# Kernel tuning notes

Measured on AMD Instinct MI355X. Metric: run time of the kernel, lower is better.

The kernel has to match this reference:

```python
import jax, jax.numpy as jnp
import numpy as np

EPS = 1e-5
K = 16

gelu = lambda x: jax.nn.gelu(x, approximate=False)

def _ln(x, g, b):
    mu = jnp.mean(x, -1, keepdims=True)
    var = jnp.mean((x - mu) ** 2, -1, keepdims=True)
    return (x - mu) * jax.lax.rsqrt(var + EPS) * g + b

def _bn_last(x, g, b, m, v):  # BN over channels-last axis (eval mode, running stats)
    return (x - m) * jax.lax.rsqrt(v + EPS) * g + b

def _bn_c(x, g, b, m, v):  # x [B,C,T]
    return (x - m[None, :, None]) * jax.lax.rsqrt(v + EPS)[None, :, None] * g[None, :, None] + b[None, :, None]

def _conv1d(x, w, b, pad):  # x [B,C,T], w [O,I,W]
    y = jax.lax.conv_general_dilated(x, w, (1,), [(pad, pad)], dimension_numbers=('NCH', 'OIH', 'NCH'))
    return y + b[None, :, None]

def _edge_conv(x, ew1, eg1, eb1, em1, ev1, ew2, eg2, eb2, em2, ev2):
    # x: [BT,P,C]; kNN in xyz (first 3 channels), gather neighbors, edge MLP, max over k
    xyz = x[..., :3]
    sq = jnp.sum(xyz * xyz, -1)
    d = sq[:, :, None] + sq[:, None, :] - 2.0 * jnp.einsum('bpc,bqc->bpq', xyz, xyz)
    _, idx = jax.lax.top_k(-d, K)                       # k smallest distances (incl. self)
    x_j = jax.vmap(lambda xb, ib: xb[ib])(x, idx)       # [BT,P,K,C]
    x_i = jnp.broadcast_to(x[:, :, None, :], x_j.shape)
    edge = jnp.concatenate([x_i, x_j - x_i], -1)        # [BT,P,K,2C]
    h = gelu(_bn_last(jnp.einsum('bpke,oe->bpko', edge, ew1), eg1, eb1, em1, ev1))
    h = gelu(_bn_last(jnp.einsum('bpko,qo->bpkq', h, ew2), eg2, eb2, em2, ev2))
    return jnp.max(h, axis=2)                           # [BT,P,128]

def setup_inputs():
    key = jax.random.key(0)
    ks = iter(jax.random.split(key, 80))
    def r(shape, s=0.05):
        return jax.random.normal(next(ks), shape, jnp.float32) * s
    d = {}
    d['x_pt'] = jax.random.normal(next(ks), (8, 32, 256, 10), jnp.float32)
    d['x_fr'] = jax.random.normal(next(ks), (8, 32, 4), jnp.float32)
    d['ew1'] = r((64, 20), 0.1)
    d['eg1'], d['eb1'], d['em1'], d['ev1'] = jnp.ones(64), jnp.zeros(64), r((64,)), jnp.ones(64)
    d['ew2'] = r((128, 64), 0.1)
    d['eg2'], d['eb2'], d['em2'], d['ev2'] = jnp.ones(128), jnp.zeros(128), r((128,)), jnp.ones(128)
    d['p1w'], d['p1b'] = r((138, 128), 0.08), r((128,))
    d['ln1g'], d['ln1b'] = jnp.ones(128), jnp.zeros(128)
    d['p2w'], d['p2b'] = r((128, 256), 0.08), r((256,))
    d['ln2g'], d['ln2b'] = jnp.ones(256), jnp.zeros(256)
    d['f1w'], d['f1b'] = r((4, 32), 0.3), r((32,))
    d['f2w'], d['f2b'] = r((32, 64), 0.15), r((64,))
    d['projw'], d['projb'] = r((256, 576, 1), 0.04), r((256,))
    for i in (1, 2, 3, 4):
        d['c%dw' % i], d['c%db' % i] = r((256, 256, 3), 0.03), r((256,))
        d['g%d' % i], d['be%d' % i], d['m%d' % i], d['v%d' % i] = jnp.ones(256), jnp.zeros(256), r((256,)), jnp.ones(256)
    d['h1w'], d['h1b'] = r((256, 128), 0.08), r((128,))
    d['h2w'], d['h2b'] = r((128, 25), 0.08), r((25,))
    return d

def reference(x_pt, x_fr, ew1, eg1, eb1, em1, ev1, ew2, eg2, eb2, em2, ev2, p1w, p1b, ln1g, ln1b, p2w, p2b, ln2g, ln2b, f1w, f1b, f2w, f2b, projw, projb, c1w, c1b, g1, be1, m1, v1, c2w, c2b, g2, be2, m2, v2, c3w, c3b, g3, be3, m3, v3, c4w, c4b, g4, be4, m4, v4, h1w, h1b, h2w, h2b):
    B, T, P, C = x_pt.shape
    x_bt = x_pt.reshape(B * T, P, C)
    local = _edge_conv(x_bt, ew1, eg1, eb1, em1, ev1, ew2, eg2, eb2, em2, ev2)
    h = jnp.concatenate([local, x_bt], -1)              # [BT,P,138]
    h = gelu(_ln(h @ p1w + p1b, ln1g, ln1b))
    h = gelu(_ln(h @ p2w + p2b, ln2g, ln2b))
    h = h.reshape(B, T, P, 256)
    pf = jnp.concatenate([jnp.max(h, 2), jnp.mean(h, 2)], -1)  # [B,T,512]
    fr = gelu(x_fr @ f1w + f1b) @ f2w + f2b                    # [B,T,64]
    per = jnp.concatenate([pf, fr], -1)                        # [B,T,576]
    hs = jnp.transpose(per, (0, 2, 1))                         # [B,576,T]
    hs = _conv1d(hs, projw, projb, 0)
    hs = gelu(_bn_c(_conv1d(hs, c1w, c1b, 1), g1, be1, m1, v1))
    hs = hs + gelu(_bn_c(_conv1d(hs, c2w, c2b, 1), g2, be2, m2, v2))
    hs = hs + gelu(_bn_c(_conv1d(hs, c3w, c3b, 1), g3, be3, m3, v3))
    hs = hs + gelu(_bn_c(_conv1d(hs, c4w, c4b, 1), g4, be4, m4, v4))
    pooled = jnp.max(hs, -1)                                   # [B,256]
    return gelu(pooled @ h1w + h1b) @ h2w + h2b                # [B,25]
```

## Files before the change

kernel.cpp:

```cpp
#include <hip/hip_runtime.h>
#include <math.h>

#define NBT   256
#define NP    256
#define NC    10
#define KNN   16
#define NPB   8

typedef unsigned short ushort_t;
typedef unsigned char uchar_t;
typedef __attribute__((ext_vector_type(8))) short short8;
typedef __attribute__((ext_vector_type(4))) float f32x4;

__device__ __forceinline__ float gelu_f(float x) {
  return 0.5f * x * (1.0f + erff(x * 0.7071067811865476f));
}
__device__ __forceinline__ float gelu_fast(float x) {
  float u  = x * 0.7071067811865476f;
  float au = fabsf(u);
  float t  = __builtin_amdgcn_rcpf(fmaf(0.3275911f, au, 1.0f));
  float p  = fmaf(t, 1.061405429f, -1.453152027f);
  p = fmaf(t, p, 1.421413741f);
  p = fmaf(t, p, -0.284496736f);
  p = fmaf(t, p, 0.254829592f);
  p = p * t;
  float e  = __expf(-au * au);
  float er = fmaf(-p, e, 1.0f);
  er = copysignf(er, u);
  return 0.5f * x * (1.0f + er);
}
__device__ __forceinline__ ushort_t f2bf(float f) {
  unsigned u = __float_as_uint(f);
  return (ushort_t)((u + 0x7FFFu + ((u >> 16) & 1u)) >> 16);
}

__global__ __launch_bounds__(256) void knn_kernel(const float* __restrict__ x_pt,
                                                  uchar_t* __restrict__ idx) {
  __shared__ float sx[NP], sy[NP], sz[NP], ssq[NP];
  int bt = blockIdx.x >> 6;
  int p0 = (blockIdx.x & 63) * 4;
  int tid = threadIdx.x;
  const float* xb = x_pt + (size_t)bt * NP * NC;
  {
    int q = tid;
    float x0 = xb[q*NC+0], x1 = xb[q*NC+1], x2 = xb[q*NC+2];
    sx[q] = x0; sy[q] = x1; sz[q] = x2;
    ssq[q] = x0*x0 + x1*x1 + x2*x2;
  }
  __syncthreads();

  int wv = tid >> 6, lane = tid & 63;
  int p = p0 + wv;
  float px = sx[p], py = sy[p], pz = sz[p], psq = ssq[p];

  unsigned k0, k1, k2, k3;
  {
    unsigned kk[4];
#pragma unroll
    for (int c = 0; c < 4; ++c) {
      int q = lane + c*64;
      float d = psq + ssq[q] - 2.0f*(px*sx[q] + py*sy[q] + pz*sz[q]);
      d = fmaxf(d, 0.0f);
      kk[c] = (__float_as_uint(d) & 0xFFFFFF00u) | (unsigned)q;
    }
    unsigned a0 = min(kk[0], kk[1]), a1 = max(kk[0], kk[1]);
    unsigned a2 = min(kk[2], kk[3]), a3 = max(kk[2], kk[3]);
    unsigned b0 = min(a0, a2), b2 = max(a0, a2);
    unsigned b1 = min(a1, a3), b3 = max(a1, a3);
    k0 = b0; k1 = min(b1, b2); k2 = max(b1, b2); k3 = b3;
  }

  unsigned cur = k0, mykeep = 0u;
#pragma unroll
  for (int r = 0; r < 16; ++r) {
    unsigned w = cur;
    w = min(w, (unsigned)__shfl_xor((int)w, 1));
    w = min(w, (unsigned)__shfl_xor((int)w, 2));
    w = min(w, (unsigned)__shfl_xor((int)w, 4));
    w = min(w, (unsigned)__shfl_xor((int)w, 8));
    w = min(w, (unsigned)__shfl_xor((int)w, 16));
    w = min(w, (unsigned)__shfl_xor((int)w, 32));
    bool win = (cur == w);
    cur = win ? k1 : cur;
    k1  = win ? k2 : k1;
    k2  = win ? k3 : k2;
    k3  = win ? 0xFFFFFFFFu : k3;
    if (lane == r) mykeep = w;
  }
  if (lane < 16)
    idx[((size_t)bt*NP + p)*KNN + lane] = (uchar_t)(mykeep & 0xFFu);
}

__global__ __launch_bounds__(256) void featAB_kernel(const float* __restrict__ x_pt,
                                                     const float* __restrict__ ew1,
                                                     float* __restrict__ Af,
                                                     float* __restrict__ Bf) {
  int t = blockIdx.x*256 + threadIdx.x;
  int o = t & 63, p = t >> 6;
  const float* xr = x_pt + (size_t)p*NC;
  float a = 0.f, b = 0.f;
#pragma unroll
  for (int e = 0; e < NC; ++e) {
    float w1 = ew1[o*20 + e], w2 = ew1[o*20 + 10 + e];
    float xv = xr[e];
    a = fmaf(xv, w1 - w2, a);
    b = fmaf(xv, w2, b);
  }
  Af[(size_t)p*64 + o] = a;
  Bf[(size_t)p*64 + o] = b;
}

__global__ __launch_bounds__(256) void prep_kernel(
    const float* __restrict__ p1w, const float* __restrict__ p2w,
    const float* __restrict__ ew2,
    ushort_t* __restrict__ w1b, ushort_t* __restrict__ w2b,
    ushort_t* __restrict__ ew2b) {
  int i = blockIdx.x*256 + threadIdx.x;
  if (i < 21504) {
    int o = i / 168, e = i - o*168;
    w1b[i] = f2bf((e < 138) ? p1w[e*128 + o] : 0.f);
  } else if (i < 56320) {
    int j = i - 21504;
    int q = j / 136, e = j - q*136;
    w2b[j] = f2bf((e < 128) ? p2w[e*256 + q] : 0.f);
  } else {
    int m = i - 56320;
    int q = m / 72, o = m - q*72;
    ew2b[m] = f2bf((o < 64) ? ew2[q*64 + o] : 0.f);
  }
}

__global__ __launch_bounds__(256) void prep2_kernel(
    const float* __restrict__ projw,
    const float* __restrict__ cw0, const float* __restrict__ cw1,
    const float* __restrict__ cw2, const float* __restrict__ cw3,
    const float* __restrict__ cb0, const float* __restrict__ cb1,
    const float* __restrict__ cb2, const float* __restrict__ cb3,
    const float* __restrict__ cg0, const float* __restrict__ cg1,
    const float* __restrict__ cg2, const float* __restrict__ cg3,
    const float* __restrict__ be0, const float* __restrict__ be1,
    const float* __restrict__ be2, const float* __restrict__ be3,
    const float* __restrict__ cm0, const float* __restrict__ cm1,
    const float* __restrict__ cm2, const float* __restrict__ cm3,
    const float* __restrict__ cv0, const float* __restrict__ cv1,
    const float* __restrict__ cv2, const float* __restrict__ cv3,
    ushort_t* __restrict__ pjb, ushort_t* __restrict__ cwb,
    float* __restrict__ SCt, float* __restrict__ SHt) {
  const float* cwp[4] = {cw0, cw1, cw2, cw3};
  const float* cbp[4] = {cb0, cb1, cb2, cb3};
  const float* cgp[4] = {cg0, cg1, cg2, cg3};
  const float* bep[4] = {be0, be1, be2, be3};
  const float* cmp[4] = {cm0, cm1, cm2, cm3};
  const float* cvp[4] = {cv0, cv1, cv2, cv3};
  int i = blockIdx.x*256 + threadIdx.x;
  if (i < 147456) {
    pjb[i] = f2bf(projw[i]);
  } else if (i < 147456 + 786432) {
    int j = i - 147456;
    int lay = j / 196608, rem = j - lay*196608;
    int c = rem / 768, kp = rem - c*768;
    int dt = kp >> 8, cin = kp & 255;
    cwb[j] = f2bf(cwp[lay][c*768 + cin*3 + dt]);
  } else if (i < 147456 + 786432 + 1024) {
    int j = i - 147456 - 786432;
    int lay = j >> 8, c = j & 255;
    float rsv = 1.0f / sqrtf(cvp[lay][c] + 1e-5f);
    float sc = cgp[lay][c] * rsv;
    SCt[j] = sc;
    SHt[j] = (cbp[lay][c] - cmp[lay][c]) * sc + bep[lay][c];
  }
}

__global__ __launch_bounds__(256, 2) void edgeconv_kernel(
    const float* __restrict__ Af, const float* __restrict__ Bf,
    const uchar_t* __restrict__ idx, const ushort_t* __restrict__ ew2b,
    const float* __restrict__ eg1, const float* __restrict__ eb1,
    const float* __restrict__ em1, const float* __restrict__ ev1,
    const float* __restrict__ eg2, const float* __restrict__ eb2,
    const float* __restrict__ em2, const float* __restrict__ ev2,
    ushort_t* __restrict__ localfb) {
  __shared__ __align__(16) ushort_t h1s[128*72];
  __shared__ __align__(16) ushort_t w2T[128*72];
  __shared__ float sc1[64], sh1[64], sc2[128], sh2[128];
  __shared__ int idxs[128];

  int tid = threadIdx.x;
  int bid = blockIdx.x;
  int wid = (bid & 7) * 1024 + (bid >> 3);
  int p0  = wid * NPB;
  int bt  = p0 >> 8;

  for (int i = tid; i < 1152; i += 256)
    ((uint4*)w2T)[i] = ((const uint4*)ew2b)[i];
  if (tid < 128) idxs[tid] = idx[(size_t)p0*16 + tid];
  if (tid < 64) {
    float s = eg1[tid] * (1.0f / sqrtf(ev1[tid] + 1e-5f));
    sc1[tid] = s; sh1[tid] = eb1[tid] - em1[tid]*s;
  }
  if (tid >= 64 && tid < 192) {
    int q = tid - 64;
    float s = eg2[q] * (1.0f / sqrtf(ev2[q] + 1e-5f));
    sc2[q] = s; sh2[q] = eb2[q] - em2[q]*s;
  }
  __syncthreads();

  {
    int o = tid & 63, g = tid >> 6;
    float s1 = sc1[o], h1v = sh1[o];
    const float* Bbase = Bf + (size_t)bt*NP*64 + o;
#pragma unroll
    for (int pi = 0; pi < 2; ++pi) {
      int pt = g*2 + pi;
      float af = Af[((size_t)(p0+pt))*64 + o];
      ushort_t* hrow = h1s + (pt*16)*72 + o;
#pragma unroll
      for (int k = 0; k < KNN; ++k) {
        int j = idxs[pt*16 + k];
        float hv = af + Bbase[(size_t)j*64];
        hrow[k*72] = f2bf(gelu_fast(fmaf(hv, s1, h1v)));
      }
    }
  }
  __syncthreads();

  int w = tid >> 6, l = tid & 63;
  int m_lo = l & 15, kq = l >> 4;

  short8 afr[2][2];
#pragma unroll
  for (int pt = 0; pt < 2; ++pt)
#pragma unroll
    for (int ks = 0; ks < 2; ++ks)
      afr[pt][ks] = *(const short8*)&h1s[((2*w+pt)*16 + m_lo)*72 + ks*32 + kq*8];

  f32x4 acc[2][8];
#pragma unroll
  for (int pt = 0; pt < 2; ++pt)
#pragma unroll
    for (int ct = 0; ct < 8; ++ct) acc[pt][ct] = (f32x4){0.f,0.f,0.f,0.f};

#pragma unroll
  for (int ct = 0; ct < 8; ++ct) {
#pragma unroll
    for (int ks = 0; ks < 2; ++ks) {
      short8 bfr = *(const short8*)&w2T[(ct*16 + m_lo)*72 + ks*32 + kq*8];
      acc[0][ct] = __builtin_amdgcn_mfma_f32_16x16x32_bf16(afr[0][ks], bfr, acc[0][ct], 0, 0, 0);
      acc[1][ct] = __builtin_amdgcn_mfma_f32_16x16x32_bf16(afr[1][ks], bfr, acc[1][ct], 0, 0, 0);
    }
  }

#pragma unroll
  for (int pt = 0; pt < 2; ++pt) {
    int gp = p0 + 2*w + pt;
#pragma unroll
    for (int ct = 0; ct < 8; ++ct) {
      int q = ct*16 + m_lo;
      float sc = sc2[q], sh = sh2[q];
      f32x4 a = acc[pt][ct];
      float mn = INFINITY, mx = -INFINITY;
#pragma unroll
      for (int r = 0; r < 4; ++r) {
        float y = fmaf(a[r], sc, sh);
        mn = fminf(mn, y); mx = fmaxf(mx, y);
      }
      mn = fminf(mn, __shfl_xor(mn, 16));
      mn = fminf(mn, __shfl_xor(mn, 32));
      mx = fmaxf(mx, __shfl_xor(mx, 16));
      mx = fmaxf(mx, __shfl_xor(mx, 32));
      float g = gelu_fast((kq & 1) ? mx : mn);
      g = fmaxf(g, __shfl_xor(g, 16));
      if (l < 16)
        localfb[(size_t)gp*128 + q] = f2bf(g);
    }
  }
}

__global__ __launch_bounds__(256, 2) void p1p2_kernel(
    const ushort_t* __restrict__ localfb, const float* __restrict__ x_pt,
    const ushort_t* __restrict__ w1b, const ushort_t* __restrict__ w2b,
    const float* __restrict__ p1b,
    const float* __restrict__ ln1g, const float* __restrict__ ln1b,
    const float* __restrict__ p2b,
    const float* __restrict__ ln2g, const float* __restrict__ ln2b,
    float* __restrict__ pmaxb, float* __restrict__ psumb) {
  __shared__ __align__(16) ushort_t sA[64*168];
  __shared__ __align__(16) ushort_t wt[128*168];
  __shared__ float pm4[4*256], ps4[4*256];
  int blk = blockIdx.x;
  int bt = blk >> 2, ch = blk & 3;
  int tid = threadIdx.x;
  size_t gbase = (size_t)bt*NP + ch*64;

  for (int i = tid; i < 1024; i += 256) {
    int pp = i >> 4, v = i & 15;
    *(uint4*)(sA + pp*168 + v*8) =
        *(const uint4*)(localfb + (gbase+pp)*128 + v*8);
  }
  for (int i = tid; i < 64*40; i += 256) {
    int pp = i / 40, e = i - pp*40;
    ushort_t v = 0;
    if (e < 10) v = f2bf(x_pt[(gbase+pp)*NC + e]);
    sA[pp*168 + 128 + e] = v;
  }
  for (int i = tid; i < 2688; i += 256)
    ((uint4*)wt)[i] = ((const uint4*)w1b)[i];
  __syncthreads();

  int w = tid >> 6, l = tid & 63;
  int lo = l & 15, kq = l >> 4;

  short8 af1[5];
#pragma unroll
  for (int ks = 0; ks < 5; ++ks)
    af1[ks] = *(const short8*)&sA[(w*16 + lo)*168 + ks*32 + kq*8];
  f32x4 acc1[8];
#pragma unroll
  for (int ct = 0; ct < 8; ++ct) {
    float b = p1b[ct*16 + lo];
    acc1[ct] = (f32x4){b, b, b, b};
  }
#pragma unroll
  for (int ct = 0; ct < 8; ++ct) {
#pragma unroll
    for (int ks = 0; ks < 5; ++ks) {
      short8 bf = *(const short8*)&wt[(ct*16 + lo)*168 + ks*32 + kq*8];
      acc1[ct] = __builtin_amdgcn_mfma_f32_16x16x32_bf16(af1[ks], bf, acc1[ct], 0, 0, 0);
    }
  }
  __syncthreads();

  {
    float g1v[8], b1v[8];
#pragma unroll
    for (int ct = 0; ct < 8; ++ct) { g1v[ct] = ln1g[ct*16+lo]; b1v[ct] = ln1b[ct*16+lo]; }
#pragma unroll
    for (int r = 0; r < 4; ++r) {
      float s = 0.f;
#pragma unroll
      for (int ct = 0; ct < 8; ++ct) s += acc1[ct][r];
      s += __shfl_xor(s,1); s += __shfl_xor(s,2); s += __shfl_xor(s,4); s += __shfl_xor(s,8);
      float mu = s * (1.0f/128.0f);
      float s2 = 0.f;
#pragma unroll
      for (int ct = 0; ct < 8; ++ct) { float d = acc1[ct][r]-mu; s2 += d*d; }
      s2 += __shfl_xor(s2,1); s2 += __shfl_xor(s2,2); s2 += __shfl_xor(s2,4); s2 += __shfl_xor(s2,8);
      float rs = 1.0f / sqrtf(s2*(1.0f/128.0f) + 1e-5f);
      int row = w*16 + kq*4 + r;
#pragma unroll
      for (int ct = 0; ct < 8; ++ct) {
        float h = gelu_fast((acc1[ct][r]-mu)*rs*g1v[ct] + b1v[ct]);
        sA[row*168 + ct*16 + lo] = f2bf(h);
      }
    }
  }
  for (int i = tid; i < 2176; i += 256)
    ((uint4*)wt)[i] = ((const uint4*)w2b)[i];
  __syncthreads();

  short8 af2[4];
#pragma unroll
  for (int ks = 0; ks < 4; ++ks)
    af2[ks] = *(const short8*)&sA[(w*16 + lo)*168 + ks*32 + kq*8];
  f32x4 acc2[16];
#pragma unroll
  for (int ct = 0; ct < 8; ++ct) {
    float bA = p2b[ct*16 + lo], bB = p2b[128 + ct*16 + lo];
    acc2[ct]   = (f32x4){bA, bA, bA, bA};
    acc2[8+ct] = (f32x4){bB, bB, bB, bB};
  }
#pragma unroll
  for (int ct = 0; ct < 8; ++ct) {
#pragma unroll
    for (int ks = 0; ks < 4; ++ks) {
      short8 bf = *(const short8*)&wt[(ct*16 + lo)*136 + ks*32 + kq*8];
      acc2[ct] = __builtin_amdgcn_mfma_f32_16x16x32_bf16(af2[ks], bf, acc2[ct], 0, 0, 0);
    }
  }
  __syncthreads();
  for (int i = tid; i < 2176; i += 256)
    ((uint4*)wt)[i] = ((const uint4*)(w2b + 17408))[i];
  __syncthreads();
#pragma unroll
  for (int ct = 0; ct < 8; ++ct) {
#pragma unroll
    for (int ks = 0; ks < 4; ++ks) {
      short8 bf = *(const short8*)&wt[(ct*16 + lo)*136 + ks*32 + kq*8];
      acc2[8+ct] = __builtin_amdgcn_mfma_f32_16x16x32_bf16(af2[ks], bf, acc2[8+ct], 0, 0, 0);
    }
  }

  float vmax[16], vsum[16];
  {
    float g2v[16], b2v[16];
#pragma unroll
    for (int j = 0; j < 16; ++j) {
      int c = (j >= 8 ? 128 : 0) + (j & 7)*16 + lo;
      g2v[j] = ln2g[c]; b2v[j] = ln2b[c];
    }
#pragma unroll
    for (int j = 0; j < 16; ++j) { vmax[j] = -INFINITY; vsum[j] = 0.f; }
#pragma unroll
    for (int r = 0; r < 4; ++r) {
      float s = 0.f;
#pragma unroll
      for (int j = 0; j < 16; ++j) s += acc2[j][r];
      s += __shfl_xor(s,1); s += __shfl_xor(s,2); s += __shfl_xor(s,4); s += __shfl_xor(s,8);
      float mu = s * (1.0f/256.0f);
      float s2 = 0.f;
#pragma unroll
      for (int j = 0; j < 16; ++j) { float d = acc2[j][r]-mu; s2 += d*d; }
      s2 += __shfl_xor(s2,1); s2 += __shfl_xor(s2,2); s2 += __shfl_xor(s2,4); s2 += __shfl_xor(s2,8);
      float rs = 1.0f / sqrtf(s2*(1.0f/256.0f) + 1e-5f);
#pragma unroll
      for (int j = 0; j < 16; ++j) {
        float v = gelu_fast((acc2[j][r]-mu)*rs*g2v[j] + b2v[j]);
        vmax[j] = fmaxf(vmax[j], v);
        vsum[j] += v;
      }
    }
  }
#pragma unroll
  for (int j = 0; j < 16; ++j) {
    float m = vmax[j], s = vsum[j];
    m = fmaxf(m, __shfl_xor(m, 16)); m = fmaxf(m, __shfl_xor(m, 32));
    s += __shfl_xor(s, 16);          s += __shfl_xor(s, 32);
    if (l < 16) {
      int c = (j >= 8 ? 128 : 0) + (j & 7)*16 + l;
      pm4[w*256 + c] = m;
      ps4[w*256 + c] = s;
    }
  }
  __syncthreads();
  {
    int c = tid;
    float mx = fmaxf(fmaxf(pm4[c], pm4[256+c]), fmaxf(pm4[512+c], pm4[768+c]));
    float sm = ps4[c] + ps4[256+c] + ps4[512+c] + ps4[768+c];
    pmaxb[(size_t)blk*256 + c] = mx;
    psumb[(size_t)blk*256 + c] = sm;
  }
}

__global__ __launch_bounds__(256) void p1p2_reduce_kernel(
    const float* __restrict__ pmaxb, const float* __restrict__ psumb,
    const float* __restrict__ xfr, const float* __restrict__ f1w,
    const float* __restrict__ f1b, const float* __restrict__ f2w,
    const float* __restrict__ f2b, float* __restrict__ perbuf) {
  int bt = blockIdx.x, q = threadIdx.x;
  const float* mb = pmaxb + (size_t)bt*4*256 + q;
  const float* sb = psumb + (size_t)bt*4*256 + q;
  float mx = -INFINITY, sm = 0.f;
#pragma unroll
  for (int i = 0; i < 4; ++i) {
    mx = fmaxf(mx, mb[i*256]);
    sm += sb[i*256];
  }
  perbuf[(size_t)bt*576 + q] = mx;
  perbuf[(size_t)bt*576 + 256 + q] = sm * (1.0f/256.0f);

  if (q < 64) {
    float x0 = xfr[bt*4], x1 = xfr[bt*4+1], x2 = xfr[bt*4+2], x3 = xfr[bt*4+3];
    float acc = f2b[q];
#pragma unroll
    for (int e = 0; e < 32; ++e) {
      float hv = f1b[e];
      hv = fmaf(x0, f1w[e], hv);
      hv = fmaf(x1, f1w[32+e], hv);
      hv = fmaf(x2, f1w[64+e], hv);
      hv = fmaf(x3, f1w[96+e], hv);
      acc = fmaf(gelu_f(hv), f2w[e*64 + q], acc);
    }
    perbuf[(size_t)bt*576 + 512 + q] = acc;
  }
}

__global__ __launch_bounds__(512, 1) void tail_kernel(
    const float* __restrict__ perbuf,
    const ushort_t* __restrict__ pjb, const ushort_t* __restrict__ cwb,
    const float* __restrict__ projb,
    const float* __restrict__ SCt, const float* __restrict__ SHt,
    const float* __restrict__ h1w, const float* __restrict__ h1b,
    const float* __restrict__ h2w, const float* __restrict__ h2b,
    float* __restrict__ out) {
  __shared__ __align__(16) ushort_t perA[32*584];
  __shared__ __align__(16) float master[32*260];
  __shared__ __align__(16) ushort_t hsb[34*264];
  __shared__ float pooled[256], hh[128];
  int b = blockIdx.x, tid = threadIdx.x;
  int w = tid >> 6, l = tid & 63;
  int lo = l & 15, kq = l >> 4;
  int mt = w & 1, nq = w >> 1;

  for (int i = tid; i < 4608; i += 512) {
    int t = i / 144, v = i - t*144;
    float4 f4 = *(const float4*)(perbuf + ((size_t)b*32 + t)*576 + v*4);
    ushort_t* dst = perA + t*584 + v*4;
    dst[0]=f2bf(f4.x); dst[1]=f2bf(f4.y); dst[2]=f2bf(f4.z); dst[3]=f2bf(f4.w);
  }
  for (int i = tid; i < 264; i += 512) { hsb[i] = 0; hsb[33*264 + i] = 0; }
  __syncthreads();

  {
    f32x4 acc[4];
#pragma unroll
    for (int j = 0; j < 4; ++j) {
      float bb = projb[(nq*4+j)*16 + lo];
      acc[j] = (f32x4){bb, bb, bb, bb};
    }
    for (int ks = 0; ks < 18; ++ks) {
      short8 af = *(const short8*)&perA[(mt*16 + lo)*584 + ks*32 + kq*8];
#pragma unroll
      for (int j = 0; j < 4; ++j) {
        int ct = nq*4 + j;
        short8 bf = *(const short8*)&pjb[(ct*16 + lo)*576 + ks*32 + kq*8];
        acc[j] = __builtin_amdgcn_mfma_f32_16x16x32_bf16(af, bf, acc[j], 0, 0, 0);
      }
    }
#pragma unroll
    for (int j = 0; j < 4; ++j) {
      int col = (nq*4+j)*16 + lo;
#pragma unroll
      for (int r = 0; r < 4; ++r)
        master[(mt*16 + kq*4 + r)*260 + col] = acc[j][r];
    }
  }
  __syncthreads();

  for (int lay = 0; lay < 4; ++lay) {
    for (int i = tid; i < 8192; i += 512) {
      int t = i >> 8, c = i & 255;
      hsb[(t+1)*264 + c] = f2bf(master[t*260 + c]);
    }
    __syncthreads();

    f32x4 acc[4];
#pragma unroll
    for (int j = 0; j < 4; ++j) acc[j] = (f32x4){0.f,0.f,0.f,0.f};
    const ushort_t* wb = cwb + (size_t)lay*196608;
    for (int ks = 0; ks < 24; ++ks) {
      int dt = ks >> 3, cin0 = (ks & 7)*32 + kq*8;
      short8 af = *(const short8*)&hsb[(mt*16 + lo + dt)*264 + cin0];
#pragma unroll
      for (int j = 0; j < 4; ++j) {
        int ct = nq*4 + j;
        short8 bf = *(const short8*)&wb[(ct*16 + lo)*768 + ks*32 + kq*8];
        acc[j] = __builtin_amdgcn_mfma_f32_16x16x32_bf16(af, bf, acc[j], 0, 0, 0);
      }
    }
    __syncthreads();
#pragma unroll
    for (int j = 0; j < 4; ++j) {
      int col = (nq*4+j)*16 + lo;
      float sc = SCt[lay*256 + col], sh = SHt[lay*256 + col];
#pragma unroll
      for (int r = 0; r < 4; ++r) {
        int row = mt*16 + kq*4 + r;
        float y = gelu_fast(fmaf(acc[j][r], sc, sh));
        if (lay > 0) y += master[row*260 + col];
        master[row*260 + col] = y;
      }
    }
    __syncthreads();
  }

  if (tid < 256) {
    float mx = -INFINITY;
#pragma unroll 8
    for (int t = 0; t < 32; ++t) mx = fmaxf(mx, master[t*260 + tid]);
    pooled[tid] = mx;
  }
  __syncthreads();
  if (tid < 128) {
    float acc = h1b[tid];
    for (int e = 0; e < 256; ++e) acc = fmaf(pooled[e], h1w[e*128 + tid], acc);
    hh[tid] = gelu_f(acc);
  }
  __syncthreads();
  if (tid < 25) {
    float acc = h2b[tid];
    for (int e = 0; e < 128; ++e) acc = fmaf(hh[e], h2w[e*25 + tid], acc);
    out[b*25 + tid] = acc;
  }
}

extern "C" void kernel_launch(void* const* d_in, const int* in_sizes, int n_in,
                              void* d_out, int out_size, void* d_ws, size_t ws_size,
                              hipStream_t stream) {
  const float* x_pt = (const float*)d_in[0];
  const float* x_fr = (const float*)d_in[1];
  const float* ew1  = (const float*)d_in[2];
  const float* eg1  = (const float*)d_in[3];
  const float* eb1  = (const float*)d_in[4];
  const float* em1  = (const float*)d_in[5];
  const float* ev1  = (const float*)d_in[6];
  const float* ew2  = (const float*)d_in[7];
  const float* eg2  = (const float*)d_in[8];
  const float* eb2  = (const float*)d_in[9];
  const float* em2  = (const float*)d_in[10];
  const float* ev2  = (const float*)d_in[11];
  const float* p1w  = (const float*)d_in[12];
  const float* p1b  = (const float*)d_in[13];
  const float* ln1g = (const float*)d_in[14];
  const float* ln1b = (const float*)d_in[15];
  const float* p2w  = (const float*)d_in[16];
  const float* p2b  = (const float*)d_in[17];
  const float* ln2g = (const float*)d_in[18];
  const float* ln2b = (const float*)d_in[19];
  const float* f1w  = (const float*)d_in[20];
  const float* f1b  = (const float*)d_in[21];
  const float* f2w  = (const float*)d_in[22];
  const float* f2b  = (const float*)d_in[23];
  const float* projw= (const float*)d_in[24];
  const float* projb= (const float*)d_in[25];
  const float* cw[4] = {(const float*)d_in[26],(const float*)d_in[32],(const float*)d_in[38],(const float*)d_in[44]};
  const float* cb[4] = {(const float*)d_in[27],(const float*)d_in[33],(const float*)d_in[39],(const float*)d_in[45]};
  const float* cg[4] = {(const float*)d_in[28],(const float*)d_in[34],(const float*)d_in[40],(const float*)d_in[46]};
  const float* cbe[4]= {(const float*)d_in[29],(const float*)d_in[35],(const float*)d_in[41],(const float*)d_in[47]};
  const float* cm[4] = {(const float*)d_in[30],(const float*)d_in[36],(const float*)d_in[42],(const float*)d_in[48]};
  const float* cv[4] = {(const float*)d_in[31],(const float*)d_in[37],(const float*)d_in[43],(const float*)d_in[49]};
  const float* h1w  = (const float*)d_in[50];
  const float* h1b  = (const float*)d_in[51];
  const float* h2w  = (const float*)d_in[52];
  const float* h2b  = (const float*)d_in[53];
  float* out = (float*)d_out;

  char* ws = (char*)d_ws;
  uchar_t* idxw  = (uchar_t*)ws;
  float* perbuf  = (float*)ws;
  ushort_t* ew2b = (ushort_t*)(ws + 0x200000);
  ushort_t* w1b  = (ushort_t*)(ws + 0x200000 + 0x8000);
  ushort_t* w2b  = (ushort_t*)(ws + 0x200000 + 0x14000);
  ushort_t* pjb  = (ushort_t*)(ws + 0x200000 + 0x28000);
  ushort_t* cwb  = (ushort_t*)(ws + 0x200000 + 0x70000);
  float* SCt     = (float*)(ws + 0x200000 + 0x1F0000);
  float* SHt     = (float*)(ws + 0x200000 + 0x1F1000);
  float* pmaxb   = (float*)(ws + ((size_t)4  << 20));
  float* psumb   = (float*)(ws + ((size_t)6  << 20));
  float* Af      = (float*)(ws + ((size_t)12 << 20));
  float* Bfw     = (float*)(ws + ((size_t)28 << 20));
  ushort_t* localfb = (ushort_t*)(ws + ((size_t)44 << 20));

  knn_kernel<<<NBT*64, 256, 0, stream>>>(x_pt, idxw);
  featAB_kernel<<<(NBT*NP*64)/256, 256, 0, stream>>>(x_pt, ew1, Af, Bfw);
  prep_kernel<<<256, 256, 0, stream>>>(p1w, p2w, ew2, w1b, w2b, ew2b);
  prep2_kernel<<<3656, 256, 0, stream>>>(projw,
      cw[0], cw[1], cw[2], cw[3], cb[0], cb[1], cb[2], cb[3],
      cg[0], cg[1], cg[2], cg[3], cbe[0], cbe[1], cbe[2], cbe[3],
      cm[0], cm[1], cm[2], cm[3], cv[0], cv[1], cv[2], cv[3],
      pjb, cwb, SCt, SHt);
  edgeconv_kernel<<<(NBT*NP)/NPB, 256, 0, stream>>>(Af, Bfw, idxw, ew2b,
      eg1, eb1, em1, ev1, eg2, eb2, em2, ev2, localfb);
  p1p2_kernel<<<NBT*4, 256, 0, stream>>>(localfb, x_pt, w1b, w2b, p1b,
      ln1g, ln1b, p2b, ln2g, ln2b, pmaxb, psumb);
  p1p2_reduce_kernel<<<NBT, 256, 0, stream>>>(pmaxb, psumb, x_fr,
      f1w, f1b, f2w, f2b, perbuf);
  tail_kernel<<<8, 512, 0, stream>>>(perbuf, pjb, cwb, projb, SCt, SHt,
      h1w, h1b, h2w, h2b, out);
}
```

Before: 518.3 us.

## Split temporal conv tail across time chunks with halo recompute and separate pool/head kernel

The tail conv stack used to run on only 8 blocks, one per batch element. It now runs on 32 blocks, each handling an 8-step time chunk plus a 4-step halo on each side, so the four k=3 convs can be recomputed locally without any cross-block sync. Out-of-range timesteps are zeroed to reproduce the per-layer zero padding. Max-pooling and the MLP head move into a new small kernel, with the first head layer split across thread pairs. This costs one extra launch, redundant halo compute, and a global round-trip of the hidden states.

```diff
diff --git a/kernel.cpp b/kernel.cpp
--- a/kernel.cpp
+++ b/kernel.cpp
@@ -473,87 +473,94 @@
   }
 }
 
-__global__ __launch_bounds__(512, 1) void tail_kernel(
+__global__ __launch_bounds__(512, 1) void tail2_kernel(
     const float* __restrict__ perbuf,
     const ushort_t* __restrict__ pjb, const ushort_t* __restrict__ cwb,
     const float* __restrict__ projb,
     const float* __restrict__ SCt, const float* __restrict__ SHt,
-    const float* __restrict__ h1w, const float* __restrict__ h1b,
-    const float* __restrict__ h2w, const float* __restrict__ h2b,
-    float* __restrict__ out) {
-  __shared__ __align__(16) ushort_t perA[32*584];
-  __shared__ __align__(16) float master[32*260];
-  __shared__ __align__(16) ushort_t hsb[34*264];
-  __shared__ float pooled[256], hh[128];
-  int b = blockIdx.x, tid = threadIdx.x;
+    float* __restrict__ hs4) {
+  __shared__ __align__(16) ushort_t perA[16*584];
+  __shared__ __align__(16) float master[16*260];
+  __shared__ __align__(16) ushort_t hsb[18*264];
+  int blk = blockIdx.x;
+  int b = blk >> 2, chunk = blk & 3;
+  int w0 = chunk*8 - 4;
+  int tid = threadIdx.x;
   int w = tid >> 6, l = tid & 63;
   int lo = l & 15, kq = l >> 4;
-  int mt = w & 1, nq = w >> 1;
-
-  for (int i = tid; i < 4608; i += 512) {
+
+  for (int i = tid; i < 16*144; i += 512) {
     int t = i / 144, v = i - t*144;
-    float4 f4 = *(const float4*)(perbuf + ((size_t)b*32 + t)*576 + v*4);
+    int gt = w0 + t;
     ushort_t* dst = perA + t*584 + v*4;
-    dst[0]=f2bf(f4.x); dst[1]=f2bf(f4.y); dst[2]=f2bf(f4.z); dst[3]=f2bf(f4.w);
-  }
-  for (int i = tid; i < 264; i += 512) { hsb[i] = 0; hsb[33*264 + i] = 0; }
+    if (gt >= 0 && gt < 32) {
+      float4 f4 = *(const float4*)(perbuf + ((size_t)b*32 + gt)*576 + v*4);
+      dst[0]=f2bf(f4.x); dst[1]=f2bf(f4.y); dst[2]=f2bf(f4.z); dst[3]=f2bf(f4.w);
+    } else {
+      dst[0]=0; dst[1]=0; dst[2]=0; dst[3]=0;
+    }
+  }
+  for (int i = tid; i < 264; i += 512) { hsb[i] = 0; hsb[17*264 + i] = 0; }
   __syncthreads();
 
   {
-    f32x4 acc[4];
-#pragma unroll
-    for (int j = 0; j < 4; ++j) {
-      float bb = projb[(nq*4+j)*16 + lo];
+    f32x4 acc[2];
+#pragma unroll
+    for (int j = 0; j < 2; ++j) {
+      float bb = projb[(2*w+j)*16 + lo];
       acc[j] = (f32x4){bb, bb, bb, bb};
     }
     for (int ks = 0; ks < 18; ++ks) {
-      short8 af = *(const short8*)&perA[(mt*16 + lo)*584 + ks*32 + kq*8];
-#pragma unroll
-      for (int j = 0; j < 4; ++j) {
-        int ct = nq*4 + j;
-        short8 bf = *(const short8*)&pjb[(ct*16 + lo)*576 + ks*32 + kq*8];
+      short8 af = *(const short8*)&perA[lo*584 + ks*32 + kq*8];
+#pragma unroll
+      for (int j = 0; j < 2; ++j) {
+        short8 bf = *(const short8*)&pjb[((2*w+j)*16 + lo)*576 + ks*32 + kq*8];
         acc[j] = __builtin_amdgcn_mfma_f32_16x16x32_bf16(af, bf, acc[j], 0, 0, 0);
       }
     }
 #pragma unroll
-    for (int j = 0; j < 4; ++j) {
-      int col = (nq*4+j)*16 + lo;
-#pragma unroll
-      for (int r = 0; r < 4; ++r)
-        master[(mt*16 + kq*4 + r)*260 + col] = acc[j][r];
+    for (int j = 0; j < 2; ++j) {
+      int col = (2*w+j)*16 + lo;
+#pragma unroll
+      for (int r = 0; r < 4; ++r) {
+        int row = kq*4 + r;
+        int gt = w0 + row;
+        master[row*260 + col] = (gt >= 0 && gt < 32) ? acc[j][r] : 0.f;
+      }
     }
   }
   __syncthreads();
 
   for (int lay = 0; lay < 4; ++lay) {
-    for (int i = tid; i < 8192; i += 512) {
+    for (int i = tid; i < 4096; i += 512) {
       int t = i >> 8, c = i & 255;
-      hsb[(t+1)*264 + c] = f2bf(master[t*260 + c]);
+      int gt = w0 + t;
+      hsb[(t+1)*264 + c] = (gt >= 0 && gt < 32) ? f2bf(master[t*260 + c])
+                                                : (ushort_t)0;
     }
     __syncthreads();
 
-    f32x4 acc[4];
-#pragma unroll
-    for (int j = 0; j < 4; ++j) acc[j] = (f32x4){0.f,0.f,0.f,0.f};
+    f32x4 acc[2];
+#pragma unroll
+    for (int j = 0; j < 2; ++j) acc[j] = (f32x4){0.f,0.f,0.f,0.f};
     const ushort_t* wb = cwb + (size_t)lay*196608;
     for (int ks = 0; ks < 24; ++ks) {
       int dt = ks >> 3, cin0 = (ks & 7)*32 + kq*8;
-      short8 af = *(const short8*)&hsb[(mt*16 + lo + dt)*264 + cin0];
-#pragma unroll
-      for (int j = 0; j < 4; ++j) {
-        int ct = nq*4 + j;
-        short8 bf = *(const short8*)&wb[(ct*16 + lo)*768 + ks*32 + kq*8];
+      short8 af = *(const short8*)&hsb[(lo + dt)*264 + cin0];
+#pragma unroll
+      for (int j = 0; j < 2; ++j) {
+        short8 bf = *(const short8*)&wb[((2*w+j)*16 + lo)*768 + ks*32 + kq*8];
         acc[j] = __builtin_amdgcn_mfma_f32_16x16x32_bf16(af, bf, acc[j], 0, 0, 0);
       }
     }
     __syncthreads();
 #pragma unroll
-    for (int j = 0; j < 4; ++j) {
-      int col = (nq*4+j)*16 + lo;
+    for (int j = 0; j < 2; ++j) {
+      int col = (2*w+j)*16 + lo;
       float sc = SCt[lay*256 + col], sh = SHt[lay*256 + col];
 #pragma unroll
       for (int r = 0; r < 4; ++r) {
-        int row = mt*16 + kq*4 + r;
+        int row = kq*4 + r;
         float y = gelu_fast(fmaf(acc[j][r], sc, sh));
         if (lay > 0) y += master[row*260 + col];
         master[row*260 + col] = y;
@@ -562,17 +569,31 @@
     __syncthreads();
   }
 
+  for (int i = tid; i < 2048; i += 512) {
+    int t = i >> 8, c = i & 255;
+    hs4[((size_t)b*32 + chunk*8 + t)*256 + c] = master[(t+4)*260 + c];
+  }
+}
+
+__global__ __launch_bounds__(256) void poolhead_kernel(
+    const float* __restrict__ hs, const float* __restrict__ h1w,
+    const float* __restrict__ h1b, const float* __restrict__ h2w,
+    const float* __restrict__ h2b, float* __restrict__ out) {
+  __shared__ float pooled[256];
+  __shared__ float hh[128];
+  int b = blockIdx.x, tid = threadIdx.x;
+  float mx = -INFINITY;
+  for (int t = 0; t < 32; ++t)
+    mx = fmaxf(mx, hs[((size_t)b*32 + t)*256 + tid]);
+  pooled[tid] = mx;
+  __syncthreads();
   if (tid < 256) {
-    float mx = -INFINITY;
-#pragma unroll 8
-    for (int t = 0; t < 32; ++t) mx = fmaxf(mx, master[t*260 + tid]);
-    pooled[tid] = mx;
-  }
-  __syncthreads();
-  if (tid < 128) {
-    float acc = h1b[tid];
-    for (int e = 0; e < 256; ++e) acc = fmaf(pooled[e], h1w[e*128 + tid], acc);
-    hh[tid] = gelu_f(acc);
+    int o = tid >> 1, half = tid & 1;
+    float acc = half ? 0.f : h1b[o];
+    for (int e = half*128; e < half*128 + 128; ++e)
+      acc = fmaf(pooled[e], h1w[e*128 + o], acc);
+    acc += __shfl_xor(acc, 1);
+    if (half == 0 && o < 128) hh[o] = gelu_f(acc);
   }
   __syncthreads();
   if (tid < 25) {
@@ -626,6 +647,7 @@
   char* ws = (char*)d_ws;
   uchar_t* idxw  = (uchar_t*)ws;
   float* perbuf  = (float*)ws;
+  float* hs4     = (float*)(ws + 0x90000);
   ushort_t* ew2b = (ushort_t*)(ws + 0x200000);
   ushort_t* w1b  = (ushort_t*)(ws + 0x200000 + 0x8000);
   ushort_t* w2b  = (ushort_t*)(ws + 0x200000 + 0x14000);
@@ -653,6 +675,6 @@
       ln1g, ln1b, p2b, ln2g, ln2b, pmaxb, psumb);
   p1p2_reduce_kernel<<<NBT, 256, 0, stream>>>(pmaxb, psumb, x_fr,
       f1w, f1b, f2w, f2b, perbuf);
-  tail_kernel<<<8, 512, 0, stream>>>(perbuf, pjb, cwb, projb, SCt, SHt,
-      h1w, h1b, h2w, h2b, out);
-}
+  tail2_kernel<<<32, 512, 0, stream>>>(perbuf, pjb, cwb, projb, SCt, SHt, hs4);
+  poolhead_kernel<<<8, 256, 0, stream>>>(hs4, h1w, h1b, h2w, h2b, out);
+}
```

After: 465.0 us. 1.11x faster.
